# Performance work log

Measured on AMD Instinct MI355X. Metric: run time of the kernel, lower is better.

## Reference

```python
import jax, jax.numpy as jnp
import numpy as np

N, E = 100000, 1600000
F_IN, H, C = 64, 64, 40


def setup_inputs() -> dict:
    key = jax.random.key(0)
    k = jax.random.split(key, 6)
    x = jax.random.normal(k[0], (N, F_IN), jnp.float32)
    edge_index = jax.random.randint(k[1], (2, E), 0, N, jnp.int32)
    edge_weight = jax.random.uniform(k[2], (E,), jnp.float32)
    W1 = jax.random.normal(k[3], (F_IN, H), jnp.float32) / np.sqrt(F_IN)
    b1 = jnp.zeros((H,), jnp.float32)
    W2 = jax.random.normal(k[4], (H, C), jnp.float32) / np.sqrt(H)
    b2 = jnp.zeros((C,), jnp.float32)
    return {"x": x, "edge_index": edge_index, "edge_weight": edge_weight,
            "W1": W1, "b1": b1, "W2": W2, "b2": b2}


def reference(x, edge_index, edge_weight, W1, b1, W2, b2):
    # PyG GCNConv: add self-loops (weight 1), symmetric normalization
    # D^{-1/2} (A + I) D^{-1/2}, linear transform, scatter-add, bias.
    n = x.shape[0]
    src, dst = edge_index[0], edge_index[1]
    loop = jnp.arange(n, dtype=src.dtype)
    src_f = jnp.concatenate([src, loop])
    dst_f = jnp.concatenate([dst, loop])
    w_f = jnp.concatenate([edge_weight, jnp.ones((n,), edge_weight.dtype)])
    deg = jax.ops.segment_sum(w_f, dst_f, num_segments=n)
    dinv = jnp.where(deg > 0, jax.lax.rsqrt(deg), 0.0)
    norm = dinv[src_f] * w_f * dinv[dst_f]  # [E+N]

    def conv(h, W, b):
        h = h @ W                                    # [n, d_out]
        msg = h[src_f] * norm[:, None]               # gather + scale, [E+N, d_out]
        return jax.ops.segment_sum(msg, dst_f, num_segments=n) + b

    h = jax.nn.relu(conv(x, W1, b1))
    # dropout is identity in eval mode (training=False)
    h = conv(h, W2, b2)
    return jax.nn.log_softmax(h, axis=1)
```

## Files before the change

### kernel.cpp

```cpp
#include <hip/hip_runtime.h>
#include <math.h>

#define N_NODES 100000
#define N_EDGES 1600000
#define C_DIM 40
#define NGROUPS 6250

#define BSZ 256
#define NB  ((N_NODES + BSZ - 1) / BSZ)
#define EB  4096
#define NBE ((N_EDGES + EB - 1) / EB)

#define OFF_DINV 0
#define OFF_BB   100000
#define OFF_CS   100392
#define OFF_ROW  100800
#define OFF_H    200802
#define OFF_REC2 353696
#define OFF_H1P  3553696
#define OFF_H2A  6753696
#define OFF_H2B  8353696
#define OFF_AGG1 8753696

typedef float floatx4 __attribute__((ext_vector_type(4)));
typedef short shortx8 __attribute__((ext_vector_type(8)));

__device__ inline unsigned short f2bf(float f) {
    unsigned int u = __float_as_uint(f);
    u += 0x7FFF + ((u >> 16) & 1);
    return (unsigned short)(u >> 16);
}
__device__ inline float bflo(unsigned int u) { return __uint_as_float(u << 16); }
__device__ inline float bfhi(unsigned int u) { return __uint_as_float(u & 0xFFFF0000u); }

__global__ __launch_bounds__(512) void k_hist2d(const int* __restrict__ ei,
                                                int* __restrict__ H,
                                                int* __restrict__ colsum) {
    __shared__ int bins[NB];
    int t = threadIdx.x, b = blockIdx.x;
    for (int i = t; i < NB; i += 512) bins[i] = 0;
    __syncthreads();
    int base = b * EB;
    for (int i = t; i < EB; i += 512) {
        int e = base + i;
        if (e < N_EDGES) atomicAdd(&bins[ei[N_EDGES + e] >> 8], 1);
    }
    __syncthreads();
    for (int i = t; i < NB; i += 512) {
        int c = bins[i];
        H[b * NB + i] = c;
        if (c) atomicAdd(&colsum[i], c);
    }
}

__global__ __launch_bounds__(512) void k_colscan(int* __restrict__ H,
                                                 const int* __restrict__ colsum,
                                                 int* __restrict__ bucketBase,
                                                 int* __restrict__ rowStart) {
    __shared__ int sd[512];
    __shared__ int sbase;
    int t = threadIdx.x, j = blockIdx.x;
    int p = 0;
    for (int i = t; i < j; i += 512) p += colsum[i];
    sd[t] = p;
    __syncthreads();
    for (int off = 256; off > 0; off >>= 1) {
        if (t < off) sd[t] += sd[t + off];
        __syncthreads();
    }
    if (t == 0) sbase = sd[0];
    __syncthreads();
    int base = sbase;
    if (t == 0) {
        bucketBase[j] = base;
        if (j == NB - 1) { bucketBase[NB] = base + colsum[j]; rowStart[N_NODES] = N_EDGES; }
    }
    __syncthreads();
    int val = (t < NBE) ? H[t * NB + j] : 0;
    sd[t] = val;
    __syncthreads();
    for (int off = 1; off < 512; off <<= 1) {
        int v = (t >= off) ? sd[t - off] : 0;
        __syncthreads();
        sd[t] += v;
        __syncthreads();
    }
    if (t < NBE) H[t * NB + j] = base + sd[t] - val;
}

__global__ __launch_bounds__(512) void k_scatter(const int* __restrict__ ei,
                                                 const float* __restrict__ w,
                                                 const int* __restrict__ blockBase,
                                                 int2* __restrict__ rec) {
    __shared__ int bases[NB];
    __shared__ int cur[NB];
    int t = threadIdx.x, b = blockIdx.x;
    for (int i = t; i < NB; i += 512) { bases[i] = blockBase[b * NB + i]; cur[i] = 0; }
    __syncthreads();
    int base = b * EB;
    for (int i = t; i < EB; i += 512) {
        int e = base + i;
        if (e < N_EDGES) {
            int s = ei[e], d = ei[N_EDGES + e];
            float wv = w[e];
            int bin = d >> 8;
            int pos = bases[bin] + atomicAdd(&cur[bin], 1);
            rec[pos] = make_int2(s | ((d & 255) << 17), __float_as_int(wv));
        }
    }
}

__global__ __launch_bounds__(512) void k_bsort(const int* __restrict__ bucketBase,
                                               const int2* __restrict__ rec,
                                               int2* __restrict__ rec2,
                                               float* __restrict__ dinv,
                                               int* __restrict__ rowStart) {
    __shared__ int   cnt[256];
    __shared__ float wsum[256];
    __shared__ int   cur[256];
    __shared__ int   sd[512];
    int t = threadIdx.x, b = blockIdx.x;
    if (t < 256) { cnt[t] = 0; wsum[t] = 0.f; }
    __syncthreads();
    int r0 = bucketBase[b], r1 = bucketBase[b + 1];
    for (int i = r0 + t; i < r1; i += 512) {
        int2 rv = rec[i];
        int l = (rv.x >> 17) & 255;
        atomicAdd(&cnt[l], 1);
        atomicAdd(&wsum[l], __int_as_float(rv.y));
    }
    __syncthreads();
    int val = (t < 256) ? cnt[t] : 0;
    sd[t] = val;
    __syncthreads();
    for (int off = 1; off < 512; off <<= 1) {
        int v = (t >= off) ? sd[t - off] : 0;
        __syncthreads();
        sd[t] += v;
        __syncthreads();
    }
    float dloc = 0.f;
    if (t < 256) {
        int excl = sd[t] - val;
        cur[t] = excl;
        int node = b * BSZ + t;
        dloc = rsqrtf(1.f + wsum[t]);
        if (node < N_NODES) {
            rowStart[node] = r0 + excl;
            dinv[node] = dloc;
        }
    }
    __syncthreads();
    if (t < 256) wsum[t] = dloc;
    __syncthreads();
    for (int i = r0 + t; i < r1; i += 512) {
        int2 rv = rec[i];
        int l = (rv.x >> 17) & 255;
        float cpart = __int_as_float(rv.y) * wsum[l];
        int pos = r0 + atomicAdd(&cur[l], 1);
        rec2[pos] = make_int2((rv.x & 0x1FFFF) << 7, __float_as_int(cpart));
    }
}

__global__ __launch_bounds__(256) void k_mm1(const float* __restrict__ x,
                                             const float* __restrict__ W1,
                                             const float* __restrict__ dinv,
                                             unsigned short* __restrict__ h1p) {
    int t = threadIdx.x, lane = t & 63, wv = t >> 6;
    int m = lane & 15, quad = lane >> 4;
    int wid = blockIdx.x * 4 + wv, nw = gridDim.x * 4;
    shortx8 B[2][4];
#pragma unroll
    for (int kc = 0; kc < 2; ++kc)
#pragma unroll
        for (int tt = 0; tt < 4; ++tt)
#pragma unroll
            for (int j = 0; j < 8; ++j) {
                int k = kc * 32 + quad * 8 + j;
                B[kc][tt][j] = (short)f2bf(W1[k * 64 + tt * 16 + m]);
            }
    for (int g = wid; g < NGROUPS; g += nw) {
        int n0 = g * 16;
        const float* xr = x + (long)(n0 + m) * 64 + quad * 8;
        floatx4 xa = ((const floatx4*)xr)[0];
        floatx4 xb = ((const floatx4*)(xr + 4))[0];
        floatx4 xc = ((const floatx4*)(xr + 32))[0];
        floatx4 xd = ((const floatx4*)(xr + 36))[0];
        shortx8 A0, A1;
#pragma unroll
        for (int j = 0; j < 4; ++j) {
            A0[j] = (short)f2bf(xa[j]);
            A0[4 + j] = (short)f2bf(xb[j]);
            A1[j] = (short)f2bf(xc[j]);
            A1[4 + j] = (short)f2bf(xd[j]);
        }
        floatx4 acc[4];
#pragma unroll
        for (int tt = 0; tt < 4; ++tt) {
            acc[tt] = (floatx4){0.f, 0.f, 0.f, 0.f};
            acc[tt] = __builtin_amdgcn_mfma_f32_16x16x32_bf16(A0, B[0][tt], acc[tt], 0, 0, 0);
            acc[tt] = __builtin_amdgcn_mfma_f32_16x16x32_bf16(A1, B[1][tt], acc[tt], 0, 0, 0);
        }
        floatx4 dv = ((const floatx4*)(dinv + n0 + quad * 4))[0];
#pragma unroll
        for (int reg = 0; reg < 4; ++reg) {
            int node = n0 + quad * 4 + reg;
            float d = dv[reg];
#pragma unroll
            for (int tt = 0; tt < 4; ++tt)
                h1p[(long)node * 64 + tt * 16 + m] = f2bf(acc[tt][reg] * d);
        }
    }
}

__global__ __launch_bounds__(256) void k_agg1(const int* __restrict__ rowStart,
                                              const int2* __restrict__ rec2,
                                              const float* __restrict__ dinv,
                                              const unsigned short* __restrict__ h1p,
                                              float* __restrict__ agg1) {
    __shared__ int2 cache[4][80];
    int t = threadIdx.x, lane = t & 63, wv = t >> 6;
    int node = blockIdx.x * 4 + wv;
    if (node >= N_NODES) return;
    int2* wc = cache[wv];
    wc[lane] = make_int2(0, 0);
    if (lane < 16) wc[64 + lane] = make_int2(0, 0);
    const char* hb = (const char*)h1p;
    int eslot = lane >> 3;
    int c = lane & 7;
    int lo = c << 4;
    float dn = dinv[node];
    float a0=0.f,a1=0.f,a2=0.f,a3=0.f,a4=0.f,a5=0.f,a6=0.f,a7=0.f;
    float b0=0.f,b1=0.f,b2=0.f,b3=0.f,b4=0.f,b5=0.f,b6=0.f,b7=0.f;
    if (eslot == 0) {
        uint4 u = *(const uint4*)(hb + ((long)node << 7) + lo);
        a0 = bflo(u.x) * dn; a1 = bfhi(u.x) * dn;
        a2 = bflo(u.y) * dn; a3 = bfhi(u.y) * dn;
        a4 = bflo(u.z) * dn; a5 = bfhi(u.z) * dn;
        a6 = bflo(u.w) * dn; a7 = bfhi(u.w) * dn;
    }
    int s0 = rowStart[node], s1 = rowStart[node + 1];
    for (int base = s0; base < s1; base += 64) {
        int idx = base + lane;
        int2 r = make_int2(0, 0);
        if (idx < s1) r = rec2[idx];
        wc[lane] = r;
        __builtin_amdgcn_wave_barrier();
        int cnt = min(64, s1 - base);
        for (int j = 0; j < cnt; j += 24) {
            int2 e0 = wc[j + eslot];
            int2 e1 = wc[j + 8 + eslot];
            int2 e2 = wc[j + 16 + eslot];
            float w0 = __int_as_float(e0.y);
            float w1 = __int_as_float(e1.y);
            float w2 = __int_as_float(e2.y);
            uint4 q0 = *(const uint4*)(hb + e0.x + lo);
            uint4 q1 = *(const uint4*)(hb + e1.x + lo);
            uint4 q2 = *(const uint4*)(hb + e2.x + lo);
            a0 = fmaf(bflo(q0.x), w0, a0); a1 = fmaf(bfhi(q0.x), w0, a1);
            a2 = fmaf(bflo(q0.y), w0, a2); a3 = fmaf(bfhi(q0.y), w0, a3);
            a4 = fmaf(bflo(q0.z), w0, a4); a5 = fmaf(bfhi(q0.z), w0, a5);
            a6 = fmaf(bflo(q0.w), w0, a6); a7 = fmaf(bfhi(q0.w), w0, a7);
            b0 = fmaf(bflo(q1.x), w1, b0); b1 = fmaf(bfhi(q1.x), w1, b1);
            b2 = fmaf(bflo(q1.y), w1, b2); b3 = fmaf(bfhi(q1.y), w1, b3);
            b4 = fmaf(bflo(q1.z), w1, b4); b5 = fmaf(bfhi(q1.z), w1, b5);
            b6 = fmaf(bflo(q1.w), w1, b6); b7 = fmaf(bfhi(q1.w), w1, b7);
            a0 = fmaf(bflo(q2.x), w2, a0); a1 = fmaf(bfhi(q2.x), w2, a1);
            a2 = fmaf(bflo(q2.y), w2, a2); a3 = fmaf(bfhi(q2.y), w2, a3);
            a4 = fmaf(bflo(q2.z), w2, a4); a5 = fmaf(bfhi(q2.z), w2, a5);
            a6 = fmaf(bflo(q2.w), w2, a6); a7 = fmaf(bfhi(q2.w), w2, a7);
        }
        __builtin_amdgcn_wave_barrier();
    }
    a0 += b0; a1 += b1; a2 += b2; a3 += b3;
    a4 += b4; a5 += b5; a6 += b6; a7 += b7;
    a0 += __shfl_xor(a0, 8, 64); a0 += __shfl_xor(a0, 16, 64); a0 += __shfl_xor(a0, 32, 64);
    a1 += __shfl_xor(a1, 8, 64); a1 += __shfl_xor(a1, 16, 64); a1 += __shfl_xor(a1, 32, 64);
    a2 += __shfl_xor(a2, 8, 64); a2 += __shfl_xor(a2, 16, 64); a2 += __shfl_xor(a2, 32, 64);
    a3 += __shfl_xor(a3, 8, 64); a3 += __shfl_xor(a3, 16, 64); a3 += __shfl_xor(a3, 32, 64);
    a4 += __shfl_xor(a4, 8, 64); a4 += __shfl_xor(a4, 16, 64); a4 += __shfl_xor(a4, 32, 64);
    a5 += __shfl_xor(a5, 8, 64); a5 += __shfl_xor(a5, 16, 64); a5 += __shfl_xor(a5, 32, 64);
    a6 += __shfl_xor(a6, 8, 64); a6 += __shfl_xor(a6, 16, 64); a6 += __shfl_xor(a6, 32, 64);
    a7 += __shfl_xor(a7, 8, 64); a7 += __shfl_xor(a7, 16, 64); a7 += __shfl_xor(a7, 32, 64);
    if (eslot == 0) {
        float* op = agg1 + ((long)node << 6) + (c << 3);
        *(float4*)op       = make_float4(a0, a1, a2, a3);
        *(float4*)(op + 4) = make_float4(a4, a5, a6, a7);
    }
}

__global__ __launch_bounds__(256) void k_agg2(const int* __restrict__ rowStart,
                                              const int2* __restrict__ rec2,
                                              const float* __restrict__ dinv,
                                              const unsigned short* __restrict__ h2a,
                                              const unsigned short* __restrict__ h2b,
                                              const float* __restrict__ b2,
                                              float* __restrict__ out) {
    __shared__ int2 cache[4][80];
    int t = threadIdx.x, lane = t & 63, wv = t >> 6;
    int node = blockIdx.x * 4 + wv;
    if (node >= N_NODES) return;
    int2* wc = cache[wv];
    wc[lane] = make_int2(0, 0);
    if (lane < 16) wc[64 + lane] = make_int2(0, 0);
    int eslot = lane / 10;
    int c = lane - eslot * 10;
    float fscale = (eslot < 6) ? 1.f : 0.f;
    const char* gb = (c < 8) ? (const char*)h2a : (const char*)h2b;
    int sh = (c < 8) ? 1 : 3;
    int lo2 = (c < 8) ? (c << 3) : ((c - 8) << 3);
    float dn = dinv[node];
    float p0 = 0.f, p1 = 0.f, p2 = 0.f, p3 = 0.f;
    float r0a = 0.f, r1a = 0.f, r2a = 0.f, r3a = 0.f;
    if (eslot == 0) {
        uint2 u = *(const uint2*)(gb + (((long)node << 7) >> sh) + lo2);
        p0 = bflo(u.x) * dn; p1 = bfhi(u.x) * dn;
        p2 = bflo(u.y) * dn; p3 = bfhi(u.y) * dn;
    }
    int s0 = rowStart[node], s1 = rowStart[node + 1];
    for (int base = s0; base < s1; base += 64) {
        int idx = base + lane;
        int2 r = make_int2(0, 0);
        if (idx < s1) r = rec2[idx];
        wc[lane] = r;
        __builtin_amdgcn_wave_barrier();
        int cnt = min(64, s1 - base);
        for (int j = 0; j < cnt; j += 18) {
            int2 e0 = wc[j + eslot];
            int2 e1 = wc[j + 6 + eslot];
            int2 e2 = wc[j + 12 + eslot];
            float f0 = __int_as_float(e0.y) * fscale;
            float f1 = __int_as_float(e1.y) * fscale;
            float f2 = __int_as_float(e2.y) * fscale;
            uint2 u0 = *(const uint2*)(gb + (e0.x >> sh) + lo2);
            uint2 u1 = *(const uint2*)(gb + (e1.x >> sh) + lo2);
            uint2 u2 = *(const uint2*)(gb + (e2.x >> sh) + lo2);
            p0 = fmaf(bflo(u0.x), f0, p0); p1 = fmaf(bfhi(u0.x), f0, p1);
            p2 = fmaf(bflo(u0.y), f0, p2); p3 = fmaf(bfhi(u0.y), f0, p3);
            r0a = fmaf(bflo(u1.x), f1, r0a); r1a = fmaf(bfhi(u1.x), f1, r1a);
            r2a = fmaf(bflo(u1.y), f1, r2a); r3a = fmaf(bfhi(u1.y), f1, r3a);
            p0 = fmaf(bflo(u2.x), f2, p0); p1 = fmaf(bfhi(u2.x), f2, p1);
            p2 = fmaf(bflo(u2.y), f2, p2); p3 = fmaf(bfhi(u2.y), f2, p3);
        }
        __builtin_amdgcn_wave_barrier();
    }
    p0 += r0a; p1 += r1a; p2 += r2a; p3 += r3a;
    p0 += __shfl(p0, (lane + 30) & 63, 64);
    p1 += __shfl(p1, (lane + 30) & 63, 64);
    p2 += __shfl(p2, (lane + 30) & 63, 64);
    p3 += __shfl(p3, (lane + 30) & 63, 64);
    p0 = p0 + __shfl(p0, (lane + 10) & 63, 64) + __shfl(p0, (lane + 20) & 63, 64);
    p1 = p1 + __shfl(p1, (lane + 10) & 63, 64) + __shfl(p1, (lane + 20) & 63, 64);
    p2 = p2 + __shfl(p2, (lane + 10) & 63, 64) + __shfl(p2, (lane + 20) & 63, 64);
    p3 = p3 + __shfl(p3, (lane + 10) & 63, 64) + __shfl(p3, (lane + 20) & 63, 64);
    bool act = lane < 10;
    float4 bb = *(const float4*)(b2 + (c << 2));
    float v0 = act ? p0 + bb.x : -INFINITY;
    float v1 = act ? p1 + bb.y : -INFINITY;
    float v2 = act ? p2 + bb.z : -INFINITY;
    float v3 = act ? p3 + bb.w : -INFINITY;
    float m = fmaxf(fmaxf(v0, v1), fmaxf(v2, v3));
#pragma unroll
    for (int off = 8; off; off >>= 1) m = fmaxf(m, __shfl_xor(m, off, 64));
    const float LOG2E = 1.4426950408889634f;
    const float LN2   = 0.6931471805599453f;
    float s = 0.f;
    if (act) {
        s  = __builtin_amdgcn_exp2f((v0 - m) * LOG2E);
        s += __builtin_amdgcn_exp2f((v1 - m) * LOG2E);
        s += __builtin_amdgcn_exp2f((v2 - m) * LOG2E);
        s += __builtin_amdgcn_exp2f((v3 - m) * LOG2E);
    }
#pragma unroll
    for (int off = 8; off; off >>= 1) s += __shfl_xor(s, off, 64);
    float ls = m + __builtin_amdgcn_logf(s) * LN2;
    if (act) {
        *(float4*)(out + (long)node * C_DIM + (c << 2)) =
            make_float4(v0 - ls, v1 - ls, v2 - ls, v3 - ls);
    }
}

__global__ __launch_bounds__(256) void k_mm2(const float* __restrict__ agg1,
                                             const float* __restrict__ b1,
                                             const float* __restrict__ W2,
                                             const float* __restrict__ dinv,
                                             unsigned short* __restrict__ h2a,
                                             unsigned short* __restrict__ h2b) {
    int t = threadIdx.x, lane = t & 63, wv = t >> 6;
    int m = lane & 15, quad = lane >> 4;
    int wid = blockIdx.x * 4 + wv, nw = gridDim.x * 4;
    shortx8 B[2][3];
#pragma unroll
    for (int kc = 0; kc < 2; ++kc)
#pragma unroll
        for (int tt = 0; tt < 3; ++tt) {
            int n = tt * 16 + m;
#pragma unroll
            for (int j = 0; j < 8; ++j) {
                int k = kc * 32 + quad * 8 + j;
                B[kc][tt][j] = (n < C_DIM) ? (short)f2bf(W2[k * C_DIM + n]) : (short)0;
            }
        }
    floatx4 ba0 = ((const floatx4*)(b1 + quad * 8))[0];
    floatx4 ba1 = ((const floatx4*)(b1 + quad * 8 + 4))[0];
    floatx4 bb0 = ((const floatx4*)(b1 + 32 + quad * 8))[0];
    floatx4 bb1 = ((const floatx4*)(b1 + 32 + quad * 8 + 4))[0];
    for (int g = wid; g < NGROUPS; g += nw) {
        int n0 = g * 16;
        const float* xr = agg1 + (long)(n0 + m) * 64 + quad * 8;
        floatx4 xa = ((const floatx4*)xr)[0];
        floatx4 xb = ((const floatx4*)(xr + 4))[0];
        floatx4 xc = ((const floatx4*)(xr + 32))[0];
        floatx4 xd = ((const floatx4*)(xr + 36))[0];
        shortx8 A0, A1;
#pragma unroll
        for (int j = 0; j < 4; ++j) {
            A0[j]     = (short)f2bf(fmaxf(xa[j] + ba0[j], 0.f));
            A0[4 + j] = (short)f2bf(fmaxf(xb[j] + ba1[j], 0.f));
            A1[j]     = (short)f2bf(fmaxf(xc[j] + bb0[j], 0.f));
            A1[4 + j] = (short)f2bf(fmaxf(xd[j] + bb1[j], 0.f));
        }
        floatx4 acc[3];
#pragma unroll
        for (int tt = 0; tt < 3; ++tt) {
            acc[tt] = (floatx4){0.f, 0.f, 0.f, 0.f};
            acc[tt] = __builtin_amdgcn_mfma_f32_16x16x32_bf16(A0, B[0][tt], acc[tt], 0, 0, 0);
            acc[tt] = __builtin_amdgcn_mfma_f32_16x16x32_bf16(A1, B[1][tt], acc[tt], 0, 0, 0);
        }
        floatx4 dv = ((const floatx4*)(dinv + n0 + quad * 4))[0];
#pragma unroll
        for (int reg = 0; reg < 4; ++reg) {
            int node = n0 + quad * 4 + reg;
            float d = dv[reg];
            h2a[(long)node * 32 + m]      = f2bf(acc[0][reg] * d);
            h2a[(long)node * 32 + 16 + m] = f2bf(acc[1][reg] * d);
            if (m < 8)
                h2b[(long)node * 8 + m]   = f2bf(acc[2][reg] * d);
        }
    }
}

extern "C" void kernel_launch(void* const* d_in, const int* in_sizes, int n_in,
                              void* d_out, int out_size, void* d_ws, size_t ws_size,
                              hipStream_t stream) {
    const float* x  = (const float*)d_in[0];
    const int*   ei = (const int*)d_in[1];
    const float* w  = (const float*)d_in[2];
    const float* W1 = (const float*)d_in[3];
    const float* b1 = (const float*)d_in[4];
    const float* W2 = (const float*)d_in[5];
    const float* b2 = (const float*)d_in[6];
    float* out = (float*)d_out;

    float* wsf = (float*)d_ws;
    int*   wsi = (int*)d_ws;
    float* dinv       = wsf + OFF_DINV;
    int*   bucketBase = wsi + OFF_BB;
    int*   colsum     = wsi + OFF_CS;
    int*   rowStart   = wsi + OFF_ROW;
    int*   H          = wsi + OFF_H;
    int2*  rec2       = (int2*)(wsi + OFF_REC2);
    int2*  rec        = (int2*)(wsi + OFF_H1P);
    unsigned short* h1p = (unsigned short*)(wsi + OFF_H1P);
    unsigned short* h2a = (unsigned short*)(wsi + OFF_H2A);
    unsigned short* h2b = (unsigned short*)(wsi + OFF_H2B);
    float* agg1       = wsf + OFF_AGG1;

    hipMemsetAsync(colsum, 0, NB * sizeof(int), stream);
    k_hist2d<<<NBE, 512, 0, stream>>>(ei, H, colsum);
    k_colscan<<<NB, 512, 0, stream>>>(H, colsum, bucketBase, rowStart);
    k_scatter<<<NBE, 512, 0, stream>>>(ei, w, H, rec);
    k_bsort<<<NB, 512, 0, stream>>>(bucketBase, rec, rec2, dinv, rowStart);

    k_mm1<<<512, 256, 0, stream>>>(x, W1, dinv, h1p);
    k_agg1<<<(N_NODES + 3) / 4, 256, 0, stream>>>(rowStart, rec2, dinv, h1p, agg1);

    k_mm2<<<512, 256, 0, stream>>>(agg1, b1, W2, dinv, h2a, h2b);
    k_agg2<<<(N_NODES + 3) / 4, 256, 0, stream>>>(rowStart, rec2, dinv, h2a, h2b, b2, out);
}
```

Measured before the change: 251.4 us.

## Fuse edge scatter with first matmul and move source dinv into edge weights

After: 259.6 us. 1.03x slower.

```diff
diff --git a/kernel.cpp b/kernel.cpp
--- a/kernel.cpp
+++ b/kernel.cpp
@@ -10,6 +10,7 @@
 #define NB  ((N_NODES + BSZ - 1) / BSZ)
 #define EB  4096
 #define NBE ((N_EDGES + EB - 1) / EB)
+#define MMB 300
 
 #define OFF_DINV 0
 #define OFF_BB   100000
@@ -41,9 +42,22 @@
     for (int i = t; i < NB; i += 512) bins[i] = 0;
     __syncthreads();
     int base = b * EB;
-    for (int i = t; i < EB; i += 512) {
-        int e = base + i;
-        if (e < N_EDGES) atomicAdd(&bins[ei[N_EDGES + e] >> 8], 1);
+    const int4* dst4 = (const int4*)(ei + N_EDGES + base);
+    for (int i = t; i < EB / 4; i += 512) {
+        int e4 = base + i * 4;
+        if (e4 + 3 < N_EDGES) {
+            int4 d = dst4[i];
+            atomicAdd(&bins[d.x >> 8], 1);
+            atomicAdd(&bins[d.y >> 8], 1);
+            atomicAdd(&bins[d.z >> 8], 1);
+            atomicAdd(&bins[d.w >> 8], 1);
+        } else {
+#pragma unroll
+            for (int k = 0; k < 4; ++k) {
+                int e = e4 + k;
+                if (e < N_EDGES) atomicAdd(&bins[ei[N_EDGES + e] >> 8], 1);
+            }
+        }
     }
     __syncthreads();
     for (int i = t; i < NB; i += 512) {
@@ -88,87 +102,57 @@
     if (t < NBE) H[t * NB + j] = base + sd[t] - val;
 }
 
-__global__ __launch_bounds__(512) void k_scatter(const int* __restrict__ ei,
+__global__ __launch_bounds__(512) void k_scatmm1(const int* __restrict__ ei,
                                                  const float* __restrict__ w,
                                                  const int* __restrict__ blockBase,
-                                                 int2* __restrict__ rec) {
+                                                 int2* __restrict__ rec,
+                                                 const float* __restrict__ x,
+                                                 const float* __restrict__ W1,
+                                                 unsigned short* __restrict__ h1p) {
     __shared__ int bases[NB];
     __shared__ int cur[NB];
     int t = threadIdx.x, b = blockIdx.x;
-    for (int i = t; i < NB; i += 512) { bases[i] = blockBase[b * NB + i]; cur[i] = 0; }
-    __syncthreads();
-    int base = b * EB;
-    for (int i = t; i < EB; i += 512) {
-        int e = base + i;
-        if (e < N_EDGES) {
-            int s = ei[e], d = ei[N_EDGES + e];
-            float wv = w[e];
-            int bin = d >> 8;
-            int pos = bases[bin] + atomicAdd(&cur[bin], 1);
-            rec[pos] = make_int2(s | ((d & 255) << 17), __float_as_int(wv));
-        }
-    }
-}
-
-__global__ __launch_bounds__(512) void k_bsort(const int* __restrict__ bucketBase,
-                                               const int2* __restrict__ rec,
-                                               int2* __restrict__ rec2,
-                                               float* __restrict__ dinv,
-                                               int* __restrict__ rowStart) {
-    __shared__ int   cnt[256];
-    __shared__ float wsum[256];
-    __shared__ int   cur[256];
-    __shared__ int   sd[512];
-    int t = threadIdx.x, b = blockIdx.x;
-    if (t < 256) { cnt[t] = 0; wsum[t] = 0.f; }
-    __syncthreads();
-    int r0 = bucketBase[b], r1 = bucketBase[b + 1];
-    for (int i = r0 + t; i < r1; i += 512) {
-        int2 rv = rec[i];
-        int l = (rv.x >> 17) & 255;
-        atomicAdd(&cnt[l], 1);
-        atomicAdd(&wsum[l], __int_as_float(rv.y));
-    }
-    __syncthreads();
-    int val = (t < 256) ? cnt[t] : 0;
-    sd[t] = val;
-    __syncthreads();
-    for (int off = 1; off < 512; off <<= 1) {
-        int v = (t >= off) ? sd[t - off] : 0;
+    if (b < NBE) {
+        for (int i = t; i < NB; i += 512) { bases[i] = blockBase[b * NB + i]; cur[i] = 0; }
         __syncthreads();
-        sd[t] += v;
-        __syncthreads();
-    }
-    float dloc = 0.f;
-    if (t < 256) {
-        int excl = sd[t] - val;
-        cur[t] = excl;
-        int node = b * BSZ + t;
-        dloc = rsqrtf(1.f + wsum[t]);
-        if (node < N_NODES) {
-            rowStart[node] = r0 + excl;
-            dinv[node] = dloc;
-        }
-    }
-    __syncthreads();
-    if (t < 256) wsum[t] = dloc;
-    __syncthreads();
-    for (int i = r0 + t; i < r1; i += 512) {
-        int2 rv = rec[i];
-        int l = (rv.x >> 17) & 255;
-        float cpart = __int_as_float(rv.y) * wsum[l];
-        int pos = r0 + atomicAdd(&cur[l], 1);
-        rec2[pos] = make_int2((rv.x & 0x1FFFF) << 7, __float_as_int(cpart));
-    }
-}
-
-__global__ __launch_bounds__(256) void k_mm1(const float* __restrict__ x,
-                                             const float* __restrict__ W1,
-                                             const float* __restrict__ dinv,
-                                             unsigned short* __restrict__ h1p) {
-    int t = threadIdx.x, lane = t & 63, wv = t >> 6;
+        int base = b * EB;
+        const int4*   src4 = (const int4*)(ei + base);
+        const int4*   dst4 = (const int4*)(ei + N_EDGES + base);
+        const float4* wv4  = (const float4*)(w + base);
+        for (int i = t; i < EB / 4; i += 512) {
+            int e4 = base + i * 4;
+            if (e4 + 3 < N_EDGES) {
+                int4 s = src4[i];
+                int4 d = dst4[i];
+                float4 wv = wv4[i];
+                int bin, pos;
+                bin = d.x >> 8; pos = bases[bin] + atomicAdd(&cur[bin], 1);
+                rec[pos] = make_int2(s.x | ((d.x & 255) << 17), __float_as_int(wv.x));
+                bin = d.y >> 8; pos = bases[bin] + atomicAdd(&cur[bin], 1);
+                rec[pos] = make_int2(s.y | ((d.y & 255) << 17), __float_as_int(wv.y));
+                bin = d.z >> 8; pos = bases[bin] + atomicAdd(&cur[bin], 1);
+                rec[pos] = make_int2(s.z | ((d.z & 255) << 17), __float_as_int(wv.z));
+                bin = d.w >> 8; pos = bases[bin] + atomicAdd(&cur[bin], 1);
+                rec[pos] = make_int2(s.w | ((d.w & 255) << 17), __float_as_int(wv.w));
+            } else {
+#pragma unroll
+                for (int k = 0; k < 4; ++k) {
+                    int e = e4 + k;
+                    if (e < N_EDGES) {
+                        int ss = ei[e], dd = ei[N_EDGES + e];
+                        float wvv = w[e];
+                        int bin = dd >> 8;
+                        int pos = bases[bin] + atomicAdd(&cur[bin], 1);
+                        rec[pos] = make_int2(ss | ((dd & 255) << 17), __float_as_int(wvv));
+                    }
+                }
+            }
+        }
+        return;
+    }
+    int lane = t & 63, wv = t >> 6;
     int m = lane & 15, quad = lane >> 4;
-    int wid = blockIdx.x * 4 + wv, nw = gridDim.x * 4;
+    int wid = (b - NBE) * 8 + wv, nw = MMB * 8;
     shortx8 B[2][4];
 #pragma unroll
     for (int kc = 0; kc < 2; ++kc)
@@ -201,15 +185,74 @@
             acc[tt] = __builtin_amdgcn_mfma_f32_16x16x32_bf16(A0, B[0][tt], acc[tt], 0, 0, 0);
             acc[tt] = __builtin_amdgcn_mfma_f32_16x16x32_bf16(A1, B[1][tt], acc[tt], 0, 0, 0);
         }
-        floatx4 dv = ((const floatx4*)(dinv + n0 + quad * 4))[0];
 #pragma unroll
         for (int reg = 0; reg < 4; ++reg) {
             int node = n0 + quad * 4 + reg;
-            float d = dv[reg];
 #pragma unroll
             for (int tt = 0; tt < 4; ++tt)
-                h1p[(long)node * 64 + tt * 16 + m] = f2bf(acc[tt][reg] * d);
-        }
+                h1p[(long)node * 64 + tt * 16 + m] = f2bf(acc[tt][reg]);
+        }
+    }
+}
+
+__global__ __launch_bounds__(512) void k_bsortA(const int* __restrict__ bucketBase,
+                                                const int2* __restrict__ rec,
+                                                float* __restrict__ dinv,
+                                                int* __restrict__ rowStart) {
+    __shared__ int   cnt[256];
+    __shared__ float wsum[256];
+    __shared__ int   sd[512];
+    int t = threadIdx.x, b = blockIdx.x;
+    if (t < 256) { cnt[t] = 0; wsum[t] = 0.f; }
+    __syncthreads();
+    int r0 = bucketBase[b], r1 = bucketBase[b + 1];
+    for (int i = r0 + t; i < r1; i += 512) {
+        int2 rv = rec[i];
+        int l = (rv.x >> 17) & 255;
+        atomicAdd(&cnt[l], 1);
+        atomicAdd(&wsum[l], __int_as_float(rv.y));
+    }
+    __syncthreads();
+    int val = (t < 256) ? cnt[t] : 0;
+    sd[t] = val;
+    __syncthreads();
+    for (int off = 1; off < 512; off <<= 1) {
+        int v = (t >= off) ? sd[t - off] : 0;
+        __syncthreads();
+        sd[t] += v;
+        __syncthreads();
+    }
+    if (t < 256) {
+        int node = b * BSZ + t;
+        if (node < N_NODES) {
+            rowStart[node] = r0 + (sd[t] - val);
+            dinv[node] = rsqrtf(1.f + wsum[t]);
+        }
+    }
+}
+
+__global__ __launch_bounds__(512) void k_bsortB(const int* __restrict__ bucketBase,
+                                                const int* __restrict__ rowStart,
+                                                const float* __restrict__ dinv,
+                                                const int2* __restrict__ rec,
+                                                int2* __restrict__ rec2) {
+    __shared__ int   cur[256];
+    __shared__ float dd[256];
+    int t = threadIdx.x, b = blockIdx.x;
+    if (t < 256) {
+        int node = b * BSZ + t;
+        cur[t] = (node < N_NODES) ? rowStart[node] : 0;
+        dd[t]  = (node < N_NODES) ? dinv[node] : 0.f;
+    }
+    __syncthreads();
+    int r0 = bucketBase[b], r1 = bucketBase[b + 1];
+    for (int i = r0 + t; i < r1; i += 512) {
+        int2 rv = rec[i];
+        int l = (rv.x >> 17) & 255;
+        int s = rv.x & 0x1FFFF;
+        float cpart = __int_as_float(rv.y) * dd[l] * dinv[s];
+        int pos = atomicAdd(&cur[l], 1);
+        rec2[pos] = make_int2(s << 7, __float_as_int(cpart));
     }
 }
 
@@ -230,14 +273,15 @@
     int c = lane & 7;
     int lo = c << 4;
     float dn = dinv[node];
+    float dn2 = dn * dn;
     float a0=0.f,a1=0.f,a2=0.f,a3=0.f,a4=0.f,a5=0.f,a6=0.f,a7=0.f;
     float b0=0.f,b1=0.f,b2=0.f,b3=0.f,b4=0.f,b5=0.f,b6=0.f,b7=0.f;
     if (eslot == 0) {
         uint4 u = *(const uint4*)(hb + ((long)node << 7) + lo);
-        a0 = bflo(u.x) * dn; a1 = bfhi(u.x) * dn;
-        a2 = bflo(u.y) * dn; a3 = bfhi(u.y) * dn;
-        a4 = bflo(u.z) * dn; a5 = bfhi(u.z) * dn;
-        a6 = bflo(u.w) * dn; a7 = bfhi(u.w) * dn;
+        a0 = bflo(u.x) * dn2; a1 = bfhi(u.x) * dn2;
+        a2 = bflo(u.y) * dn2; a3 = bfhi(u.y) * dn2;
+        a4 = bflo(u.z) * dn2; a5 = bfhi(u.z) * dn2;
+        a6 = bflo(u.w) * dn2; a7 = bfhi(u.w) * dn2;
     }
     int s0 = rowStart[node], s1 = rowStart[node + 1];
     for (int base = s0; base < s1; base += 64) {
@@ -310,12 +354,13 @@
     int sh = (c < 8) ? 1 : 3;
     int lo2 = (c < 8) ? (c << 3) : ((c - 8) << 3);
     float dn = dinv[node];
+    float dn2 = dn * dn;
     float p0 = 0.f, p1 = 0.f, p2 = 0.f, p3 = 0.f;
     float r0a = 0.f, r1a = 0.f, r2a = 0.f, r3a = 0.f;
     if (eslot == 0) {
         uint2 u = *(const uint2*)(gb + (((long)node << 7) >> sh) + lo2);
-        p0 = bflo(u.x) * dn; p1 = bfhi(u.x) * dn;
-        p2 = bflo(u.y) * dn; p3 = bfhi(u.y) * dn;
+        p0 = bflo(u.x) * dn2; p1 = bfhi(u.x) * dn2;
+        p2 = bflo(u.y) * dn2; p3 = bfhi(u.y) * dn2;
     }
     int s0 = rowStart[node], s1 = rowStart[node + 1];
     for (int base = s0; base < s1; base += 64) {
@@ -383,7 +428,6 @@
 __global__ __launch_bounds__(256) void k_mm2(const float* __restrict__ agg1,
                                              const float* __restrict__ b1,
                                              const float* __restrict__ W2,
-                                             const float* __restrict__ dinv,
                                              unsigned short* __restrict__ h2a,
                                              unsigned short* __restrict__ h2b) {
     int t = threadIdx.x, lane = t & 63, wv = t >> 6;
@@ -427,15 +471,13 @@
             acc[tt] = __builtin_amdgcn_mfma_f32_16x16x32_bf16(A0, B[0][tt], acc[tt], 0, 0, 0);
             acc[tt] = __builtin_amdgcn_mfma_f32_16x16x32_bf16(A1, B[1][tt], acc[tt], 0, 0, 0);
         }
-        floatx4 dv = ((const floatx4*)(dinv + n0 + quad * 4))[0];
 #pragma unroll
         for (int reg = 0; reg < 4; ++reg) {
             int node = n0 + quad * 4 + reg;
-            float d = dv[reg];
-            h2a[(long)node * 32 + m]      = f2bf(acc[0][reg] * d);
-            h2a[(long)node * 32 + 16 + m] = f2bf(acc[1][reg] * d);
+            h2a[(long)node * 32 + m]      = f2bf(acc[0][reg]);
+            h2a[(long)node * 32 + 16 + m] = f2bf(acc[1][reg]);
             if (m < 8)
-                h2b[(long)node * 8 + m]   = f2bf(acc[2][reg] * d);
+                h2b[(long)node * 8 + m]   = f2bf(acc[2][reg]);
         }
     }
 }
@@ -460,7 +502,7 @@
     int*   rowStart   = wsi + OFF_ROW;
     int*   H          = wsi + OFF_H;
     int2*  rec2       = (int2*)(wsi + OFF_REC2);
-    int2*  rec        = (int2*)(wsi + OFF_H1P);
+    int2*  rec        = (int2*)(wsi + OFF_AGG1);
     unsigned short* h1p = (unsigned short*)(wsi + OFF_H1P);
     unsigned short* h2a = (unsigned short*)(wsi + OFF_H2A);
     unsigned short* h2b = (unsigned short*)(wsi + OFF_H2B);
@@ -469,12 +511,12 @@
     hipMemsetAsync(colsum, 0, NB * sizeof(int), stream);
     k_hist2d<<<NBE, 512, 0, stream>>>(ei, H, colsum);
     k_colscan<<<NB, 512, 0, stream>>>(H, colsum, bucketBase, rowStart);
-    k_scatter<<<NBE, 512, 0, stream>>>(ei, w, H, rec);
-    k_bsort<<<NB, 512, 0, stream>>>(bucketBase, rec, rec2, dinv, rowStart);
-
-    k_mm1<<<512, 256, 0, stream>>>(x, W1, dinv, h1p);
+    k_scatmm1<<<NBE + MMB, 512, 0, stream>>>(ei, w, H, rec, x, W1, h1p);
+    k_bsortA<<<NB, 512, 0, stream>>>(bucketBase, rec, dinv, rowStart);
+    k_bsortB<<<NB, 512, 0, stream>>>(bucketBase, rowStart, dinv, rec, rec2);
+
     k_agg1<<<(N_NODES + 3) / 4, 256, 0, stream>>>(rowStart, rec2, dinv, h1p, agg1);
 
-    k_mm2<<<512, 256, 0, stream>>>(agg1, b1, W2, dinv, h2a, h2b);
+    k_mm2<<<512, 256, 0, stream>>>(agg1, b1, W2, h2a, h2b);
     k_agg2<<<(N_NODES + 3) / 4, 256, 0, stream>>>(rowStart, rec2, dinv, h2a, h2b, b2, out);
 }
```
